# Kernel optimization log

Measured on AMD Instinct MI355X. Metric: run time of the kernel, lower is better.

## Reference

```python
import jax, jax.numpy as jnp
import numpy as np

N_NODES = 100000
N_EDGES = 1600000
IN_DIM = 128
HID = 64
OUT_DIM = 3


def _glorot(key, shape):
    fan_in, fan_out = shape[0], shape[1]
    std = (2.0 / (fan_in + fan_out)) ** 0.5
    return jax.random.normal(key, shape, jnp.float32) * std


def setup_inputs() -> dict:
    key = jax.random.key(0)
    ks = jax.random.split(key, 12)
    x = jax.random.normal(ks[0], (N_NODES, IN_DIM), jnp.float32)
    edge_index = jax.random.randint(ks[1], (2, N_EDGES), 0, N_NODES, dtype=jnp.int32)
    return {
        "x": x,
        "edge_index": edge_index,
        "W1": _glorot(ks[2], (IN_DIM, HID)), "b1": jnp.zeros((HID,), jnp.float32),
        "W2": _glorot(ks[3], (HID, HID)), "b2": jnp.zeros((HID,), jnp.float32),
        "W3": _glorot(ks[4], (HID, HID)), "b3": jnp.zeros((HID,), jnp.float32),
        "W4": _glorot(ks[5], (HID, HID // 2)), "b4": jnp.zeros((HID // 2,), jnp.float32),
        "Wh": _glorot(ks[6], (HID // 2, OUT_DIM)), "bh": jnp.zeros((OUT_DIM,), jnp.float32),
    }


def reference(x, edge_index, W1, b1, W2, b2, W3, b3, W4, b4, Wh, bh):
    n = x.shape[0]
    self_loops = jnp.arange(n, dtype=edge_index.dtype)
    src = jnp.concatenate([edge_index[0], self_loops])  # message sources j
    dst = jnp.concatenate([edge_index[1], self_loops])  # aggregation targets i
    # symmetric GCN normalization with self-loops: deg over targets (unit edge weights)
    deg = jax.ops.segment_sum(jnp.ones_like(dst, jnp.float32), dst, num_segments=n)
    dinv = jnp.where(deg > 0, jax.lax.rsqrt(deg), 0.0)
    norm = dinv[src] * dinv[dst]  # [E+N]

    def gcn(h, W, b):
        h = h @ W  # transform first (PyG GCNConv order)
        agg = jax.ops.segment_sum(h[src] * norm[:, None], dst, num_segments=n)
        return agg + b

    h = jax.nn.relu(gcn(x, W1, b1))   # dropout is identity in eval mode
    h = jax.nn.relu(gcn(h, W2, b2))
    h = jax.nn.relu(gcn(h, W3, b3))
    h = jax.nn.relu(gcn(h, W4, b4))
    return h @ Wh + bh  # [N, 3]
```

## Files before the change

### kernel.cpp

```cpp
#include <hip/hip_runtime.h>
#include <hip/hip_bf16.h>
#include <hip/hip_fp16.h>
#include <cstdint>


#define MAXD 512
#define EB   8192
#define PADSLACK 2048

typedef _Float16 half8v __attribute__((ext_vector_type(8)));
typedef _Float16 half2v __attribute__((ext_vector_type(2)));
typedef float    float4v __attribute__((ext_vector_type(4)));

#if defined(__has_builtin)
#if __has_builtin(__builtin_amdgcn_fdot2)
#define HAVE_FDOT2 1
#endif
#endif

__device__ __forceinline__ float fdot2f(half2v a, half2v b, float c) {
#ifdef HAVE_FDOT2
    return __builtin_amdgcn_fdot2(a, b, c, false);
#else
    return c + (float)a[0] * (float)b[0] + (float)a[1] * (float)b[1];
#endif
}

__device__ __forceinline__ void hist_body(const int* __restrict__ ei,
                                          int* __restrict__ histM, int E, int b) {
    __shared__ int hist[MAXD];
    const int tid = threadIdx.x;
    hist[tid] = 0; hist[tid + 256] = 0;
    __syncthreads();
    const int base = b * EB;
#pragma unroll 2
    for (int it = 0; it < EB / 256; it += 4) {
        int d[4]; bool ok[4];
#pragma unroll
        for (int u = 0; u < 4; ++u) {
            int e = base + (it + u) * 256 + tid;
            ok[u] = e < E;
            d[u] = ok[u] ? ei[E + e] : 0;
        }
#pragma unroll
        for (int u = 0; u < 4; ++u)
            if (ok[u]) atomicAdd(&hist[d[u] >> 8], 1);
    }
    __syncthreads();
    histM[(size_t)b * MAXD + tid] = hist[tid];
    histM[(size_t)b * MAXD + tid + 256] = hist[tid + 256];
}

__global__ __launch_bounds__(256) void scan_digits_k(int* __restrict__ histM,
                                                     int* __restrict__ totals,
                                                     int NBLK) {
    __shared__ int s[256];
    const int t = threadIdx.x, dg = blockIdx.x;
    int v = (t < NBLK) ? histM[(size_t)t * MAXD + dg] : 0;
    s[t] = v;
    __syncthreads();
    for (int off = 1; off < 256; off <<= 1) {
        int x = (t >= off) ? s[t - off] : 0;
        __syncthreads();
        s[t] += x;
        __syncthreads();
    }
    if (t < NBLK) histM[(size_t)t * MAXD + dg] = s[t] - v;
    if (t == 255) totals[dg] = s[255];
}

__global__ __launch_bounds__(512) void scan_base_k(const int* __restrict__ totals,
                                                   int* __restrict__ cb, int ND) {
    __shared__ int s[512];
    const int t = threadIdx.x;
    int v = (t < ND) ? totals[t] : 0;
    s[t] = v;
    __syncthreads();
    for (int off = 1; off < 512; off <<= 1) {
        int x = (t >= off) ? s[t - off] : 0;
        __syncthreads();
        s[t] += x;
        __syncthreads();
    }
    if (t < ND) cb[t] = s[t] - v;
    if (t == 511) cb[ND] = s[511];
}

template <int K, int OUT>
__device__ __forceinline__ void gemm_body(const float* __restrict__ H,
                                          const float* __restrict__ W,
                                          float* __restrict__ Tout, int n, int bx) {
    constexpr int TX  = OUT / 4;
    constexpr int TY  = 256 / TX;
    constexpr int BM  = TY * 4;
    constexpr int BK  = 32;
    constexpr int PAD = 4;

    __shared__ float At[BK][BM + PAD];
    __shared__ float Ws[BK][OUT];

    const int t    = threadIdx.x;
    const int cx   = t % TX;
    const int ry   = t / TX;
    const int row0 = bx * BM;

    float acc[4][4] = {{0.f}};
    const int arow = t >> 3;
    const int af4  = t & 7;

    for (int k0 = 0; k0 < K; k0 += BK) {
#pragma unroll
        for (int p = 0; p < BM / 32; ++p) {
            int r  = arow + p * 32;
            int gr = row0 + r;
            int grc = gr < n ? gr : n - 1;
            float4 v = *reinterpret_cast<const float4*>(
                H + (size_t)grc * K + k0 + af4 * 4);
            At[af4 * 4 + 0][r] = v.x;
            At[af4 * 4 + 1][r] = v.y;
            At[af4 * 4 + 2][r] = v.z;
            At[af4 * 4 + 3][r] = v.w;
        }
#pragma unroll
        for (int p = 0; p < (BK * OUT) / 1024; ++p) {
            int idx = t + p * 256;
            int wk  = idx / (OUT / 4);
            int wf  = idx % (OUT / 4);
            float4 v = *reinterpret_cast<const float4*>(
                W + (size_t)(k0 + wk) * OUT + wf * 4);
            *reinterpret_cast<float4*>(&Ws[wk][wf * 4]) = v;
        }
        __syncthreads();
#pragma unroll
        for (int k = 0; k < BK; ++k) {
            float4 a = *reinterpret_cast<const float4*>(&At[k][ry * 4]);
            float4 w = *reinterpret_cast<const float4*>(&Ws[k][cx * 4]);
            acc[0][0] = fmaf(a.x, w.x, acc[0][0]);
            acc[0][1] = fmaf(a.x, w.y, acc[0][1]);
            acc[0][2] = fmaf(a.x, w.z, acc[0][2]);
            acc[0][3] = fmaf(a.x, w.w, acc[0][3]);
            acc[1][0] = fmaf(a.y, w.x, acc[1][0]);
            acc[1][1] = fmaf(a.y, w.y, acc[1][1]);
            acc[1][2] = fmaf(a.y, w.z, acc[1][2]);
            acc[1][3] = fmaf(a.y, w.w, acc[1][3]);
            acc[2][0] = fmaf(a.z, w.x, acc[2][0]);
            acc[2][1] = fmaf(a.z, w.y, acc[2][1]);
            acc[2][2] = fmaf(a.z, w.z, acc[2][2]);
            acc[2][3] = fmaf(a.z, w.w, acc[2][3]);
            acc[3][0] = fmaf(a.w, w.x, acc[3][0]);
            acc[3][1] = fmaf(a.w, w.y, acc[3][1]);
            acc[3][2] = fmaf(a.w, w.z, acc[3][2]);
            acc[3][3] = fmaf(a.w, w.w, acc[3][3]);
        }
        __syncthreads();
    }
#pragma unroll
    for (int i = 0; i < 4; ++i) {
        int gr = row0 + ry * 4 + i;
        if (gr < n) {
            float4 v = make_float4(acc[i][0], acc[i][1], acc[i][2], acc[i][3]);
            *reinterpret_cast<float4*>(Tout + (size_t)gr * OUT + cx * 4) = v;
        }
    }
}

__device__ __forceinline__ void pack_body(const int* __restrict__ ei,
                                          const int* __restrict__ histM,
                                          const int* __restrict__ cb,
                                          int* __restrict__ packed,
                                          int E, int ND, int b) {
    __shared__ int cur[MAXD];
    const int tid = threadIdx.x;
    for (int t = tid; t < ND; t += 256)
        cur[t] = cb[t] + histM[(size_t)b * MAXD + t];
    __syncthreads();
    const int base = b * EB;
    for (int it = 0; it < EB / 256; it += 4) {
        int s[4], d[4]; bool ok[4];
#pragma unroll
        for (int u = 0; u < 4; ++u) {
            int e = base + (it + u) * 256 + tid;
            ok[u] = e < E;
            if (ok[u]) { s[u] = ei[e]; d[u] = ei[E + e]; }
        }
#pragma unroll
        for (int u = 0; u < 4; ++u) {
            if (ok[u]) {
                int pos = atomicAdd(&cur[d[u] >> 8], 1);
                packed[pos] = (s[u] << 8) | (d[u] & 255);
            }
        }
    }
}

__global__ __launch_bounds__(256) void hist_gemm1_k(
    const int* __restrict__ ei, int* __restrict__ histM, int E,
    const float* __restrict__ x, const float* __restrict__ W1,
    float* __restrict__ T1, int n, int NH) {
    const int bx = blockIdx.x;
    if (bx < NH) hist_body(ei, histM, E, bx);
    else         gemm_body<128, 64>(x, W1, T1, n, bx - NH);
}

__global__ __launch_bounds__(256) void pack_gemm1_k(
    const int* __restrict__ ei, const int* __restrict__ histM,
    const int* __restrict__ cb, int* __restrict__ packed,
    const float* __restrict__ x, const float* __restrict__ W1,
    float* __restrict__ T1, int n, int E, int ND, int NPB, int G1) {
    const int bx = blockIdx.x;
    if (bx < NPB) pack_body(ei, histM, cb, packed, E, ND, bx);
    else          gemm_body<128, 64>(x, W1, T1, n, G1 + bx - NPB);
}

__global__ __launch_bounds__(256) void bucket_k(const int* __restrict__ packed,
                                                const int* __restrict__ cb,
                                                int* __restrict__ col,
                                                int* __restrict__ rowptr,
                                                int* __restrict__ counts,
                                                float* __restrict__ dinv,
                                                const float* __restrict__ Traw,
                                                __half* __restrict__ Th, int n) {
    __shared__ int   hist[256];
    __shared__ int   pref[256];
    __shared__ int   cur[256];
    __shared__ float dinv_l[256];

    const int tid   = threadIdx.x;
    const int dg    = blockIdx.x;
    const int base  = cb[dg];
    const int m     = cb[dg + 1] - base;
    const int basep = base + dg * PADSLACK;

    hist[tid] = 0;
    __syncthreads();
    for (int k0 = 0; k0 < m; k0 += 1024) {
        int v[4]; bool ok[4];
#pragma unroll
        for (int u = 0; u < 4; ++u) {
            int k = k0 + u * 256 + tid;
            ok[u] = k < m;
            v[u] = ok[u] ? packed[base + k] : 0;
        }
#pragma unroll
        for (int u = 0; u < 4; ++u)
            if (ok[u]) atomicAdd(&hist[v[u] & 255], 1);
    }
    __syncthreads();
    const int deg   = hist[tid];
    const int cnt_p = (deg + 8) & ~7;
    pref[tid] = cnt_p;
    __syncthreads();
    for (int off = 1; off < 256; off <<= 1) {
        int x = (tid >= off) ? pref[tid - off] : 0;
        __syncthreads();
        pref[tid] += x;
        __syncthreads();
    }
    const int rp = basep + pref[tid] - cnt_p;
    const float di = rsqrtf((float)(deg + 1));
    dinv_l[tid] = di;
    cur[tid] = rp + 1;
    const int d = dg * 256 + tid;
    if (d < n) {
        counts[d] = cnt_p;
        dinv[d]   = di;
        rowptr[d] = rp;
        col[rp]   = d;
        for (int k = deg + 1; k < cnt_p; ++k) col[rp + k] = n;
    }
    __syncthreads();
    for (int k0 = 0; k0 < m; k0 += 1024) {
        int v[4]; bool ok[4];
#pragma unroll
        for (int u = 0; u < 4; ++u) {
            int k = k0 + u * 256 + tid;
            ok[u] = k < m;
            v[u] = ok[u] ? packed[base + k] : 0;
        }
#pragma unroll
        for (int u = 0; u < 4; ++u) {
            if (ok[u]) {
                int pos = atomicAdd(&cur[v[u] & 255], 1);
                col[pos] = v[u] >> 8;
            }
        }
    }
    const int r0 = dg * 256;
#pragma unroll 4
    for (int it = 0; it < 16; ++it) {
        int idx = it * 256 + tid;
        int rl  = idx >> 4;
        int r   = r0 + rl;
        if (r < n) {
            float4 v = reinterpret_cast<const float4*>(Traw)[(size_t)r * 16 + (idx & 15)];
            float dd = dinv_l[rl];
            union { ushort4 u; __half h[4]; } pk;
            pk.h[0] = __float2half_rn(v.x * dd);
            pk.h[1] = __float2half_rn(v.y * dd);
            pk.h[2] = __float2half_rn(v.z * dd);
            pk.h[3] = __float2half_rn(v.w * dd);
            reinterpret_cast<ushort4*>(Th)[(size_t)r * 16 + (idx & 15)] = pk.u;
        }
    }
    if (dg == 0 && tid < 16) {
        uint2 z; z.x = 0u; z.y = 0u;
        reinterpret_cast<uint2*>(Th)[(size_t)n * 16 + tid] = z;
    }
}

template <int OUT>
__global__ __launch_bounds__(256) void gemm_mfma_k(
    const _Float16* __restrict__ H, const float* __restrict__ W,
    const float* __restrict__ dinv, _Float16* __restrict__ T, int n) {
    constexpr int NT = OUT / 16;
    const int lane = threadIdx.x & 63;
    const int m16  = lane & 15;
    const int quad = lane >> 4;
    const int wid  = (blockIdx.x * blockDim.x + threadIdx.x) >> 6;
    const int nw   = (gridDim.x * blockDim.x) >> 6;

    half8v bfrag[NT][2];
#pragma unroll
    for (int t = 0; t < NT; ++t)
#pragma unroll
        for (int h = 0; h < 2; ++h)
#pragma unroll
            for (int j = 0; j < 8; ++j)
                bfrag[t][h][j] = (_Float16)W[(size_t)(h * 32 + quad * 8 + j) * OUT
                                             + t * 16 + m16];

    const int nblk = (n + 15) >> 4;
    for (int rb = wid; rb < nblk; rb += nw) {
        const int r0 = rb * 16;
        int ra = r0 + m16; if (ra >= n) ra = n - 1;
        const half8v* hrow = reinterpret_cast<const half8v*>(H + (size_t)ra * 64);
        half8v a0 = hrow[quad];
        half8v a1 = hrow[4 + quad];

        float4v dfr[NT];
#pragma unroll
        for (int t = 0; t < NT; ++t) {
            float4v z = {0.f, 0.f, 0.f, 0.f};
            z = __builtin_amdgcn_mfma_f32_16x16x32_f16(a0, bfrag[t][0], z, 0, 0, 0);
            z = __builtin_amdgcn_mfma_f32_16x16x32_f16(a1, bfrag[t][1], z, 0, 0, 0);
            dfr[t] = z;
        }
#pragma unroll
        for (int reg = 0; reg < 4; ++reg) {
            int row = r0 + quad * 4 + reg;
            if (row < n) {
                float di = dinv[row];
#pragma unroll
                for (int t = 0; t < NT; ++t)
                    T[(size_t)row * 64 + t * 16 + m16] =
                        (_Float16)(dfr[t][reg] * di);
            }
        }
    }
}

template <int LR, bool FUSE_HEAD>
__global__ __launch_bounds__(256) void agg_k(const __half* __restrict__ T,
                                             const int* __restrict__ rowptr,
                                             const int* __restrict__ counts,
                                             const int* __restrict__ col,
                                             const float* __restrict__ dinv,
                                             const float* __restrict__ bias,
                                             void* __restrict__ O, int n,
                                             const float* __restrict__ Wh,
                                             const float* __restrict__ bh) {
    constexpr int NSW = 64 / LR;
    constexpr int U   = 16 / NSW;
    constexpr int UH  = U / 2;
    const int lane = threadIdx.x & 63;
    const int q    = lane % LR;
    const int sw   = lane / LR;
    const int i = (blockIdx.x * blockDim.x + threadIdx.x) >> 6;
    if (i >= n) return;

    const half2v s10 = {(_Float16)1.f, (_Float16)0.f};
    const half2v s01 = {(_Float16)0.f, (_Float16)1.f};

    const int start = rowptr[i];
    const int cnt   = counts[i];
    const uint2* __restrict__ T2 = reinterpret_cast<const uint2*>(T);

    float4 acc = make_float4(0.f, 0.f, 0.f, 0.f);
    for (int base = 0; base < cnt; base += 64) {
        const int m = min(64, cnt - base);
        int c_l = col[start + base + lane];
        int jg = 0;
        for (; jg + 16 <= m; jg += 16) {
            int cc[U]; uint2 v[U];
#pragma unroll
            for (int u = 0; u < U; ++u)
                cc[u] = __shfl(c_l, jg + u * NSW + sw, 64);
#pragma unroll
            for (int u = 0; u < U; ++u) v[u] = T2[(size_t)cc[u] * 16 + q];
#pragma unroll
            for (int u = 0; u < U; ++u) {
                union { uint2 uu; half2v h[2]; } cv; cv.uu = v[u];
                acc.x = fdot2f(cv.h[0], s10, acc.x);
                acc.y = fdot2f(cv.h[0], s01, acc.y);
                acc.z = fdot2f(cv.h[1], s10, acc.z);
                acc.w = fdot2f(cv.h[1], s01, acc.w);
            }
        }
        if (jg < m) {
            int cc[UH]; uint2 v[UH];
#pragma unroll
            for (int u = 0; u < UH; ++u)
                cc[u] = __shfl(c_l, jg + u * NSW + sw, 64);
#pragma unroll
            for (int u = 0; u < UH; ++u) v[u] = T2[(size_t)cc[u] * 16 + q];
#pragma unroll
            for (int u = 0; u < UH; ++u) {
                union { uint2 uu; half2v h[2]; } cv; cv.uu = v[u];
                acc.x = fdot2f(cv.h[0], s10, acc.x);
                acc.y = fdot2f(cv.h[0], s01, acc.y);
                acc.z = fdot2f(cv.h[1], s10, acc.z);
                acc.w = fdot2f(cv.h[1], s01, acc.w);
            }
        }
    }
#pragma unroll
    for (int off = LR; off < 64; off <<= 1) {
        acc.x += __shfl_xor(acc.x, off, 64);
        acc.y += __shfl_xor(acc.y, off, 64);
        acc.z += __shfl_xor(acc.z, off, 64);
        acc.w += __shfl_xor(acc.w, off, 64);
    }
    const float di = dinv[i];
    const float4 b4 = reinterpret_cast<const float4*>(bias)[q];
    float4 h;
    h.x = fmaxf(fmaf(di, acc.x, b4.x), 0.f);
    h.y = fmaxf(fmaf(di, acc.y, b4.y), 0.f);
    h.z = fmaxf(fmaf(di, acc.z, b4.z), 0.f);
    h.w = fmaxf(fmaf(di, acc.w, b4.w), 0.f);
    if constexpr (!FUSE_HEAD) {
        if (sw == 0) {
            union { ushort4 u; __half hh[4]; } pk;
            pk.hh[0] = __float2half_rn(h.x);
            pk.hh[1] = __float2half_rn(h.y);
            pk.hh[2] = __float2half_rn(h.z);
            pk.hh[3] = __float2half_rn(h.w);
            ushort* base_p = (ushort*)O + (size_t)i * 64;
            *reinterpret_cast<ushort4*>(base_p + 4 * q) = pk.u;
        }
    } else {
        float* Of = (float*)O;
        float p0 = h.x * Wh[(4 * q + 0) * 3 + 0];
        float p1 = h.x * Wh[(4 * q + 0) * 3 + 1];
        float p2 = h.x * Wh[(4 * q + 0) * 3 + 2];
        p0 = fmaf(h.y, Wh[(4 * q + 1) * 3 + 0], p0);
        p1 = fmaf(h.y, Wh[(4 * q + 1) * 3 + 1], p1);
        p2 = fmaf(h.y, Wh[(4 * q + 1) * 3 + 2], p2);
        p0 = fmaf(h.z, Wh[(4 * q + 2) * 3 + 0], p0);
        p1 = fmaf(h.z, Wh[(4 * q + 2) * 3 + 1], p1);
        p2 = fmaf(h.z, Wh[(4 * q + 2) * 3 + 2], p2);
        p0 = fmaf(h.w, Wh[(4 * q + 3) * 3 + 0], p0);
        p1 = fmaf(h.w, Wh[(4 * q + 3) * 3 + 1], p1);
        p2 = fmaf(h.w, Wh[(4 * q + 3) * 3 + 2], p2);
#pragma unroll
        for (int off = 1; off < LR; off <<= 1) {
            p0 += __shfl_xor(p0, off, 64);
            p1 += __shfl_xor(p1, off, 64);
            p2 += __shfl_xor(p2, off, 64);
        }
        if (lane == 0) {
            Of[(size_t)i * 3 + 0] = p0 + bh[0];
            Of[(size_t)i * 3 + 1] = p1 + bh[1];
            Of[(size_t)i * 3 + 2] = p2 + bh[2];
        }
    }
}

extern "C" void kernel_launch(void* const* d_in, const int* in_sizes, int n_in,
                              void* d_out, int out_size, void* d_ws, size_t ws_size,
                              hipStream_t stream) {
    const float* x  = (const float*)d_in[0];
    const int*   ei = (const int*)d_in[1];
    const float* W1 = (const float*)d_in[2];
    const float* b1 = (const float*)d_in[3];
    const float* W2 = (const float*)d_in[4];
    const float* b2 = (const float*)d_in[5];
    const float* W3 = (const float*)d_in[6];
    const float* b3 = (const float*)d_in[7];
    const float* W4 = (const float*)d_in[8];
    const float* b4 = (const float*)d_in[9];
    const float* Wh = (const float*)d_in[10];
    const float* bh = (const float*)d_in[11];
    float* out = (float*)d_out;

    const int n = in_sizes[0] / 128;
    const int E = in_sizes[1] / 2;
    const int ND   = (n + 255) / 256;
    const int NBLK = (E + EB - 1) / EB;

    char* ws = (char*)d_ws;
    auto alloc = [&](size_t bytes) {
        char* p = ws;
        ws += (bytes + 255) & ~(size_t)255;
        return p;
    };
    int*    histM  = (int*)alloc((size_t)NBLK * MAXD * 4);
    int*    totals = (int*)alloc((size_t)MAXD * 4);
    int*    cbA    = (int*)alloc((size_t)(MAXD + 1) * 4);
    int*    packed = (int*)alloc((size_t)E * 4);
    int*    col    = (int*)alloc(((size_t)E + (size_t)ND * PADSLACK + 256) * 4);
    int*    rowptr = (int*)alloc((size_t)n * 4);
    int*    counts = (int*)alloc((size_t)n * 4);
    float*  dinv   = (float*)alloc((size_t)n * 4);
    float*  bufF   = (float*)alloc((size_t)n * 64 * 4);
    __half* bufH   = (__half*)alloc(((size_t)n + 1) * 64 * 2);
    __half* bufG   = (__half*)bufF;

    dim3 blk(256);
    const int G  = (n + 63) / 64;
    const int G1 = G / 3;
    const int G2 = G - G1;
    const int agg_blocks = (n + 3) / 4;
    const int mfma_blocks = 640;

    hist_gemm1_k<<<dim3(NBLK + G1), blk, 0, stream>>>(ei, histM, E, x, W1, bufF, n, NBLK);
    scan_digits_k<<<dim3(ND), blk, 0, stream>>>(histM, totals, NBLK);
    scan_base_k<<<dim3(1), dim3(512), 0, stream>>>(totals, cbA, ND);
    pack_gemm1_k<<<dim3(NBLK + G2), blk, 0, stream>>>(ei, histM, cbA, packed,
                                                      x, W1, bufF, n, E, ND, NBLK, G1);
    bucket_k<<<dim3(ND), blk, 0, stream>>>(packed, cbA, col, rowptr, counts,
                                           dinv, bufF, bufH, n);
    agg_k<16, false><<<dim3(agg_blocks), blk, 0, stream>>>(
        bufH, rowptr, counts, col, dinv, b1, bufG, n, nullptr, nullptr);
    gemm_mfma_k<64><<<dim3(mfma_blocks), blk, 0, stream>>>(
        (const _Float16*)bufG, W2, dinv, (_Float16*)bufH, n);
    agg_k<16, false><<<dim3(agg_blocks), blk, 0, stream>>>(
        bufH, rowptr, counts, col, dinv, b2, bufG, n, nullptr, nullptr);
    gemm_mfma_k<64><<<dim3(mfma_blocks), blk, 0, stream>>>(
        (const _Float16*)bufG, W3, dinv, (_Float16*)bufH, n);
    agg_k<16, false><<<dim3(agg_blocks), blk, 0, stream>>>(
        bufH, rowptr, counts, col, dinv, b3, bufG, n, nullptr, nullptr);
    gemm_mfma_k<32><<<dim3(mfma_blocks), blk, 0, stream>>>(
        (const _Float16*)bufG, W4, dinv, (_Float16*)bufH, n);
    agg_k<8, true><<<dim3(agg_blocks), blk, 0, stream>>>(
        bufH, rowptr, counts, col, dinv, b4, out, n, Wh, bh);
}
```

Before: 365.7 us.

## Fold digit-base scan into pack/bucket kernels and add short-row aggregation path

Removes the single-block scan_base_k launch. Each pack and bucket block now recomputes the prefix over the digit totals itself in shared memory, which drops one kernel launch and one dependency at the cost of redundant per-block scan work. The aggregation kernel also gains a fast path for rows with at most 64 neighbours. That path issues all gathers in groups of 8 before accumulating, for more memory-level parallelism, and the general path now uses 8-edge granularity. The padding relies on col being padded to multiples of 8, which the bucket layout appears to provide.

```diff
diff --git a/kernel.cpp b/kernel.cpp
--- a/kernel.cpp
+++ b/kernel.cpp
@@ -24,6 +24,26 @@
 #else
     return c + (float)a[0] * (float)b[0] + (float)a[1] * (float)b[1];
 #endif
+}
+
+__device__ __forceinline__ void digit_base_scan(const int* __restrict__ totals,
+                                                int ND, int* pairs, int* cbs) {
+    const int t = threadIdx.x;
+    const int e0 = 2 * t, e1 = 2 * t + 1;
+    int v0 = (e0 < ND) ? totals[e0] : 0;
+    int v1 = (e1 < ND) ? totals[e1] : 0;
+    pairs[t] = v0 + v1;
+    __syncthreads();
+    for (int off = 1; off < 256; off <<= 1) {
+        int x = (t >= off) ? pairs[t - off] : 0;
+        __syncthreads();
+        pairs[t] += x;
+        __syncthreads();
+    }
+    int ep = pairs[t] - v0 - v1;
+    cbs[e0] = ep;
+    cbs[e1] = ep + v0;
+    __syncthreads();
 }
 
 __device__ __forceinline__ void hist_body(const int* __restrict__ ei,
@@ -67,23 +87,6 @@
     }
     if (t < NBLK) histM[(size_t)t * MAXD + dg] = s[t] - v;
     if (t == 255) totals[dg] = s[255];
-}
-
-__global__ __launch_bounds__(512) void scan_base_k(const int* __restrict__ totals,
-                                                   int* __restrict__ cb, int ND) {
-    __shared__ int s[512];
-    const int t = threadIdx.x;
-    int v = (t < ND) ? totals[t] : 0;
-    s[t] = v;
-    __syncthreads();
-    for (int off = 1; off < 512; off <<= 1) {
-        int x = (t >= off) ? s[t - off] : 0;
-        __syncthreads();
-        s[t] += x;
-        __syncthreads();
-    }
-    if (t < ND) cb[t] = s[t] - v;
-    if (t == 511) cb[ND] = s[511];
 }
 
 template <int K, int OUT>
@@ -166,13 +169,16 @@
 
 __device__ __forceinline__ void pack_body(const int* __restrict__ ei,
                                           const int* __restrict__ histM,
-                                          const int* __restrict__ cb,
+                                          const int* __restrict__ totals,
                                           int* __restrict__ packed,
                                           int E, int ND, int b) {
+    __shared__ int pairs[256];
+    __shared__ int cbs[MAXD];
     __shared__ int cur[MAXD];
     const int tid = threadIdx.x;
+    digit_base_scan(totals, ND, pairs, cbs);
     for (int t = tid; t < ND; t += 256)
-        cur[t] = cb[t] + histM[(size_t)b * MAXD + t];
+        cur[t] = cbs[t] + histM[(size_t)b * MAXD + t];
     __syncthreads();
     const int base = b * EB;
     for (int it = 0; it < EB / 256; it += 4) {
@@ -204,31 +210,35 @@
 
 __global__ __launch_bounds__(256) void pack_gemm1_k(
     const int* __restrict__ ei, const int* __restrict__ histM,
-    const int* __restrict__ cb, int* __restrict__ packed,
+    const int* __restrict__ totals, int* __restrict__ packed,
     const float* __restrict__ x, const float* __restrict__ W1,
     float* __restrict__ T1, int n, int E, int ND, int NPB, int G1) {
     const int bx = blockIdx.x;
-    if (bx < NPB) pack_body(ei, histM, cb, packed, E, ND, bx);
+    if (bx < NPB) pack_body(ei, histM, totals, packed, E, ND, bx);
     else          gemm_body<128, 64>(x, W1, T1, n, G1 + bx - NPB);
 }
 
 __global__ __launch_bounds__(256) void bucket_k(const int* __restrict__ packed,
-                                                const int* __restrict__ cb,
+                                                const int* __restrict__ totals,
+                                                int ND,
                                                 int* __restrict__ col,
                                                 int* __restrict__ rowptr,
                                                 int* __restrict__ counts,
                                                 float* __restrict__ dinv,
                                                 const float* __restrict__ Traw,
                                                 __half* __restrict__ Th, int n) {
+    __shared__ int   pairs[256];
+    __shared__ int   cbs[MAXD];
     __shared__ int   hist[256];
     __shared__ int   pref[256];
     __shared__ int   cur[256];
     __shared__ float dinv_l[256];
 
-    const int tid   = threadIdx.x;
-    const int dg    = blockIdx.x;
-    const int base  = cb[dg];
-    const int m     = cb[dg + 1] - base;
+    const int tid = threadIdx.x;
+    const int dg  = blockIdx.x;
+    digit_base_scan(totals, ND, pairs, cbs);
+    const int base  = cbs[dg];
+    const int m     = totals[dg];
     const int basep = base + dg * PADSLACK;
 
     hist[tid] = 0;
@@ -370,8 +380,7 @@
                                              const float* __restrict__ Wh,
                                              const float* __restrict__ bh) {
     constexpr int NSW = 64 / LR;
-    constexpr int U   = 16 / NSW;
-    constexpr int UH  = U / 2;
+    constexpr int GPE = 8 / NSW;
     const int lane = threadIdx.x & 63;
     const int q    = lane % LR;
     const int sw   = lane / LR;
@@ -386,40 +395,52 @@
     const uint2* __restrict__ T2 = reinterpret_cast<const uint2*>(T);
 
     float4 acc = make_float4(0.f, 0.f, 0.f, 0.f);
-    for (int base = 0; base < cnt; base += 64) {
-        const int m = min(64, cnt - base);
-        int c_l = col[start + base + lane];
-        int jg = 0;
-        for (; jg + 16 <= m; jg += 16) {
-            int cc[U]; uint2 v[U];
-#pragma unroll
-            for (int u = 0; u < U; ++u)
-                cc[u] = __shfl(c_l, jg + u * NSW + sw, 64);
-#pragma unroll
-            for (int u = 0; u < U; ++u) v[u] = T2[(size_t)cc[u] * 16 + q];
-#pragma unroll
-            for (int u = 0; u < U; ++u) {
-                union { uint2 uu; half2v h[2]; } cv; cv.uu = v[u];
-                acc.x = fdot2f(cv.h[0], s10, acc.x);
-                acc.y = fdot2f(cv.h[0], s01, acc.y);
-                acc.z = fdot2f(cv.h[1], s10, acc.z);
-                acc.w = fdot2f(cv.h[1], s01, acc.w);
+    if (cnt <= 64) {
+        int c_l = col[start + lane];
+        const int nb = cnt >> 3;
+        uint2 v[8 * GPE];
+#pragma unroll
+        for (int g = 0; g < 8; ++g) {
+            if (g < nb) {
+#pragma unroll
+                for (int u = 0; u < GPE; ++u) {
+                    int cc = __shfl(c_l, g * 8 + u * NSW + sw, 64);
+                    v[g * GPE + u] = T2[(size_t)cc * 16 + q];
+                }
             }
         }
-        if (jg < m) {
-            int cc[UH]; uint2 v[UH];
-#pragma unroll
-            for (int u = 0; u < UH; ++u)
-                cc[u] = __shfl(c_l, jg + u * NSW + sw, 64);
-#pragma unroll
-            for (int u = 0; u < UH; ++u) v[u] = T2[(size_t)cc[u] * 16 + q];
-#pragma unroll
-            for (int u = 0; u < UH; ++u) {
-                union { uint2 uu; half2v h[2]; } cv; cv.uu = v[u];
-                acc.x = fdot2f(cv.h[0], s10, acc.x);
-                acc.y = fdot2f(cv.h[0], s01, acc.y);
-                acc.z = fdot2f(cv.h[1], s10, acc.z);
-                acc.w = fdot2f(cv.h[1], s01, acc.w);
+#pragma unroll
+        for (int g = 0; g < 8; ++g) {
+            if (g < nb) {
+#pragma unroll
+                for (int u = 0; u < GPE; ++u) {
+                    union { uint2 uu; half2v h[2]; } cv; cv.uu = v[g * GPE + u];
+                    acc.x = fdot2f(cv.h[0], s10, acc.x);
+                    acc.y = fdot2f(cv.h[0], s01, acc.y);
+                    acc.z = fdot2f(cv.h[1], s10, acc.z);
+                    acc.w = fdot2f(cv.h[1], s01, acc.w);
+                }
+            }
+        }
+    } else {
+        for (int base = 0; base < cnt; base += 64) {
+            const int m = min(64, cnt - base);
+            int c_l = col[start + base + lane];
+            for (int jg = 0; jg < m; jg += 8) {
+                int cc[GPE]; uint2 v[GPE];
+#pragma unroll
+                for (int u = 0; u < GPE; ++u)
+                    cc[u] = __shfl(c_l, jg + u * NSW + sw, 64);
+#pragma unroll
+                for (int u = 0; u < GPE; ++u) v[u] = T2[(size_t)cc[u] * 16 + q];
+#pragma unroll
+                for (int u = 0; u < GPE; ++u) {
+                    union { uint2 uu; half2v h[2]; } cv; cv.uu = v[u];
+                    acc.x = fdot2f(cv.h[0], s10, acc.x);
+                    acc.y = fdot2f(cv.h[0], s01, acc.y);
+                    acc.z = fdot2f(cv.h[1], s10, acc.z);
+                    acc.w = fdot2f(cv.h[1], s01, acc.w);
+                }
             }
         }
     }
@@ -505,7 +526,6 @@
     };
     int*    histM  = (int*)alloc((size_t)NBLK * MAXD * 4);
     int*    totals = (int*)alloc((size_t)MAXD * 4);
-    int*    cbA    = (int*)alloc((size_t)(MAXD + 1) * 4);
     int*    packed = (int*)alloc((size_t)E * 4);
     int*    col    = (int*)alloc(((size_t)E + (size_t)ND * PADSLACK + 256) * 4);
     int*    rowptr = (int*)alloc((size_t)n * 4);
@@ -524,10 +544,9 @@
 
     hist_gemm1_k<<<dim3(NBLK + G1), blk, 0, stream>>>(ei, histM, E, x, W1, bufF, n, NBLK);
     scan_digits_k<<<dim3(ND), blk, 0, stream>>>(histM, totals, NBLK);
-    scan_base_k<<<dim3(1), dim3(512), 0, stream>>>(totals, cbA, ND);
-    pack_gemm1_k<<<dim3(NBLK + G2), blk, 0, stream>>>(ei, histM, cbA, packed,
+    pack_gemm1_k<<<dim3(NBLK + G2), blk, 0, stream>>>(ei, histM, totals, packed,
                                                       x, W1, bufF, n, E, ND, NBLK, G1);
-    bucket_k<<<dim3(ND), blk, 0, stream>>>(packed, cbA, col, rowptr, counts,
+    bucket_k<<<dim3(ND), blk, 0, stream>>>(packed, totals, ND, col, rowptr, counts,
                                            dinv, bufF, bufH, n);
     agg_k<16, false><<<dim3(agg_blocks), blk, 0, stream>>>(
         bufH, rowptr, counts, col, dinv, b1, bufG, n, nullptr, nullptr);
```

Result: no change. 363.9 us (-0.5%).
